# Optimization experiments

Hardware: AMD Instinct MI355X
Metric: run time of the kernel (lower is better)

## Reference

```python
import jax, jax.numpy as jnp
import numpy as np

T = 2_097_152  # timesteps


def setup_inputs() -> dict:
    key = jax.random.key(0)
    # precipitation P and potential evapotranspiration E, in mm/day
    x = jax.random.uniform(key, (T, 2), dtype=jnp.float32) * 10.0
    x1 = jnp.float32(350.0)  # production store capacity (mm)
    return {"x": x, "x1": x1}


def reference(x, x1):
    # GR4J production storage. s_init = 0.0.
    P = x[:, 0]
    E = x[:, 1]
    p_n = jax.nn.relu(P - E)  # net rainfall
    e_n = jax.nn.relu(E - P)  # net evapotranspiration
    # tanh(p_n/x1), tanh(e_n/x1) only depend on inputs -> precompute (same math)
    t_p = jnp.tanh(p_n / x1)
    t_e = jnp.tanh(e_n / x1)
    s0 = jnp.float32(0.0) * x1  # s_init * x1

    def step(s, te):
        tp, tn = te
        r = s / x1
        p_s = x1 * (1.0 - r ** 2) * tp / (1.0 + r * tp)
        e_s = s * (2.0 - r) * tn / (1.0 + (1.0 - r) * tn)
        s = s + p_s - e_s
        perc = s * (1.0 - (1.0 + ((4.0 / 9.0) * s / x1) ** 4) ** (-0.25))
        s = s - perc
        return s, (p_s, perc, s)

    _, (p_s, perc, s_store) = jax.lax.scan(step, s0, (t_p, t_e))

    # concat([p_n[:,None], e_n[:,None], p_s[:,None], perc[:,None]], axis=1)
    out = jnp.stack([p_n, e_n, p_s, perc], axis=1)  # [T, 4]
    # scale=True with mu/sigma None: standardize with batch statistics
    mu = jnp.mean(out, axis=0)
    sigma = jnp.std(out, axis=0)  # population std, matches tf.math.reduce_std
    out = (out - mu) / sigma
    return out, s_store[:, None]
```

## Files before the change

kernel.cpp:

```cpp
#include <hip/hip_runtime.h>


typedef float f32x4 __attribute__((ext_vector_type(4)));

#define LCH      64
#define CPB      128
#define TPB      256
#define BSTEPS   8192
#define WUP      1408
#define WUPAIR   704
#define WST      88
#define NPAIRW   4768
#define NCW      151
#define DASLOT   (32*NCW)
#define NCK      129
#define NMST     8

#define CC1 0.98078528f
#define CC2 0.92387953f
#define CC3 0.83146961f
#define CC4 0.70710678f
#define CC5 0.55557023f
#define CC6 0.38268343f
#define CC7 0.19509032f

__device__ __forceinline__ void stepk(float& s, const f32x4 k, float gma) {
    float s2m = s * s;
    float t1  = fmaf(k.y, s, k.x);
    float t2  = fmaf(k.w, s, k.z);
    float s1  = fmaf(s2m, t2, t1);
    float w2  = s1 * s1;
    float q4  = gma * s1;
    float w4  = w2 * w2;
    s = fmaf(-q4, w4, s1);
}

__device__ __forceinline__ void stepk_m(float& s, const f32x4 k, float gma,
                                        float& ps_o, float& pc_o) {
    float sp  = s;
    float s2m = s * s;
    float t1  = fmaf(k.y, s, k.x);
    float t2  = fmaf(k.w, s, k.z);
    float s1  = fmaf(s2m, t2, t1);
    float w2  = s1 * s1;
    float q4  = gma * s1;
    float w4  = w2 * w2;
    s = fmaf(-q4, w4, s1);
    ps_o = fmaxf(s1 - sp, 0.0f);
    pc_o = q4 * w4;
}

struct KC { float inv, x1, x1sq, x1_2, two_x1cu, five_x1sq, four_x1; };

__device__ __forceinline__ f32x4 mkk(float P, float Ev, const KC c,
                                     float& pn_o, float& en_o) {
    float d  = P - Ev;
    float pn = fmaxf(d, 0.f), en = fmaxf(-d, 0.f);
    float up = pn * c.inv, un = en * c.inv;
    float tp = up * fmaf(up * up, -(1.f/3.f), 1.f);
    float tn = un * fmaf(un * un, -(1.f/3.f), 1.f);
    float al = tp * c.inv, be = tn * c.inv;
    float a2 = al * al,  a3v = a2 * al;
    float b2 = be * be,  b3v = b2 * be;
    float e2 = fmaf(-be, c.x1, 1.f);
    float k0 = tp * c.x1;
    float k1 = 1.f - a2 * c.x1sq - (c.x1_2 * be * e2 + c.two_x1cu * b3v);
    float k2 = (a3v * c.x1sq - al) - (c.x1_2 * b2 - be * e2 - c.five_x1sq * b3v);
    float k3 = a2 + b2 - c.four_x1 * b3v;
    pn_o = pn; en_o = en;
    return (f32x4){k0, k1, k2, k3};
}

__global__ __launch_bounds__(256, 1) void scan_pair(
        const float* __restrict__ x, const float* __restrict__ x1p,
        f32x4* __restrict__ pspc4, f32x4* __restrict__ s4,
        float* __restrict__ partials) {
    __shared__ f32x4 smem[2 * DASLOT];
    __shared__ float red[32];
    f32x4* const dA = smem;
    f32x4* const dB = smem + DASLOT;
    f32x4* const tk = smem;

    const int tid  = threadIdx.x;
    const int lane = tid & 63;
    const int wid  = tid >> 6;
    const int b    = blockIdx.x;

    const float x1 = x1p[0];
    KC c;
    c.inv = 1.0f / x1; c.x1 = x1; c.x1sq = x1 * x1; c.x1_2 = 2.0f * x1;
    c.two_x1cu = 2.0f * x1 * c.x1sq; c.five_x1sq = 5.0f * c.x1sq;
    c.four_x1 = 4.0f * x1;
    const float gma = 64.0f / (6561.0f * c.x1sq * c.x1sq);
    const float cen = (184.0f / 350.0f) * x1;
    const float hw  = (208.0f / 350.0f) * x1;
    const float ihw = 1.0f / hw;

    float snode[8];
    {
        const float ND[8] = { CC1,  CC3,  CC5,  CC7, -CC7, -CC5, -CC3, -CC1};
        #pragma unroll
        for (int j = 0; j < 8; ++j) snode[j] = fmaf(hw, ND[j], cen);
    }
    f32x4 padA, padB;
    {
        const float qq = -2.0f * gma * ihw;
        const float c2_ = cen * cen, c3_ = c2_ * cen, c4_ = c2_ * c2_, c5_ = c4_ * cen;
        const float h2 = hw * hw, h3 = h2 * hw, h4 = h2 * h2, h5 = h4 * hw;
        padA = (f32x4){qq * c5_, fmaf(qq, 5.0f * hw * c4_, 1.0f),
                       qq * 10.0f * h2 * c3_, qq * 10.0f * h3 * c2_};
        padB = (f32x4){qq * 5.0f * h4 * cen, qq * h5, 0.0f, 0.0f};
    }

    {
        const f32x4* __restrict__ x4 = (const f32x4*)x;
        const long Bb = (long)b * 4096 - WUPAIR;
        const f32x4 z4 = (f32x4){0.f, 0.f, 0.f, 0.f};
        long g0 = Bb + tid;
        f32x4 w = (tid < NPAIRW && g0 >= 0) ? x4[g0] : z4;
        #pragma unroll 1
        for (int m = 0; m < 19; ++m) {
            const int p  = tid + (m << 8);
            const int p2 = p + 256;
            const long g  = Bb + p;
            const long g2 = Bb + p2;
            f32x4 wn = (p2 < NPAIRW && g2 >= 0) ? x4[g2] : z4;
            if (p < NPAIRW) {
                f32x4 ra, rb;
                if (g < 0) { ra = padA; rb = padB; }
                else {
                    float du0, du1;
                    const f32x4 kA = mkk(w.x, w.y, c, du0, du1);
                    const f32x4 kB = mkk(w.z, w.w, c, du0, du1);
                    float v[8];
                    #pragma unroll
                    for (int j = 0; j < 8; ++j) {
                        float s = snode[j];
                        stepk(s, kA, gma);
                        stepk(s, kB, gma);
                        v[j] = (s - cen) * ihw;
                    }
                    const float e0 = v[0] + v[7], e1 = v[1] + v[6];
                    const float e2 = v[2] + v[5], e3 = v[3] + v[4];
                    const float o0 = v[0] - v[7], o1 = v[1] - v[6];
                    const float o2 = v[2] - v[5], o3 = v[3] - v[4];
                    const float a0 = 0.125f * (e0 + e1 + e2 + e3);
                    const float a1 = 0.25f * (o0*CC1 + o1*CC3 + o2*CC5 + o3*CC7);
                    const float a2 = 0.25f * ((e0 - e3)*CC2 + (e1 - e2)*CC6);
                    const float a3 = 0.25f * (o0*CC3 - o1*CC7 - o2*CC1 - o3*CC5);
                    const float a4 = 0.25f * CC4 * ((e0 + e3) - (e1 + e2));
                    const float a5 = 0.25f * (o0*CC5 - o1*CC1 + o2*CC7 + o3*CC3);
                    const float a6 = 0.25f * ((e0 - e3)*CC6 - (e1 - e2)*CC2);
                    const float a7 = 0.25f * (o0*CC7 - o1*CC5 + o2*CC3 - o3*CC1);
                    ra = (f32x4){a0 - a2 + a4 - a6,
                                 a1 - 3.0f*a3 + 5.0f*a5 - 7.0f*a7,
                                 2.0f*a2 - 8.0f*a4 + 18.0f*a6,
                                 4.0f*a3 - 20.0f*a5 + 56.0f*a7};
                    rb = (f32x4){8.0f*a4 - 48.0f*a6,
                                 16.0f*a5 - 112.0f*a7,
                                 32.0f*a6,
                                 64.0f*a7};
                }
                const int slot = (p & 31) * NCW + (p >> 5);
                dA[slot] = ra;
                dB[slot] = rb;
            }
            w = wn;
        }
    }
    __syncthreads();

    float aps = 0.f, apc = 0.f, qps = 0.f, qpc = 0.f;
    float sg = 0.f;
    if (tid < CPB) {
        const int l = tid;
        const long chk = (long)b * CPB + l;
        const float s0 = (chk * LCH >= WUP) ? 0.47f * x1 : 0.0f;
        sg = (s0 - cen) * ihw;
        f32x4 PA[8], PB[8], QA[8], QB[8];
        auto rdw = [&](f32x4 (&A)[8], f32x4 (&B)[8], const int st) {
            const int jb = st << 3;
            const int base = (jb & 31) * NCW + l + (jb >> 5);
            #pragma unroll
            for (int u = 0; u < 8; ++u) A[u] = dA[base + u * NCW];
            #pragma unroll
            for (int u = 0; u < 8; ++u) B[u] = dB[base + u * NCW];
        };
        auto wstp = [&](f32x4 (&A)[8], f32x4 (&B)[8]) {
            #pragma unroll
            for (int u = 0; u < 8; ++u) {
                const float s2  = sg * sg;
                const float p0  = fmaf(A[u].y, sg, A[u].x);
                const float p1  = fmaf(A[u].w, sg, A[u].z);
                const float p2  = fmaf(B[u].y, sg, B[u].x);
                const float p3  = fmaf(B[u].w, sg, B[u].z);
                const float s4v = s2 * s2;
                const float q0  = fmaf(p1, s2, p0);
                const float q1  = fmaf(p3, s2, p2);
                sg = fmaf(q1, s4v, q0);
            }
        };
        rdw(PA, PB, 0);
        #pragma unroll 1
        for (int st = 0; st < WST; st += 2) {
            rdw(QA, QB, st + 1);
            wstp(PA, PB);
            rdw(PA, PB, st + 2);
            wstp(QA, QB);
        }
    }
    const float s_after = fmaf(hw, sg, cen);
    __syncthreads();

    float spn = 0.f, sen = 0.f, qpn = 0.f, qen = 0.f;
    {
        const f32x4* __restrict__ x4 = (const f32x4*)x;
        const long Fb = (long)b * 4096;
        f32x4 w = x4[Fb + tid];
        #pragma unroll 1
        for (int m = 0; m < 16; ++m) {
            const int f = tid + (m << 8);
            f32x4 wn = (m < 15) ? x4[Fb + f + 256] : w;
            #pragma unroll
            for (int h = 0; h < 2; ++h) {
                float pn, en;
                const f32x4 k = mkk(h ? w.z : w.x, h ? w.w : w.y, c, pn, en);
                const int t = 2 * f + h;
                tk[(t & 63) * NCK + (t >> 6)] = k;
                spn += pn; sen += en;
                qpn = fmaf(pn, pn, qpn); qen = fmaf(en, en, qen);
            }
            w = wn;
        }
    }
    __syncthreads();

    if (tid < CPB) {
        const int l = tid;
        const size_t chunk = (size_t)b * CPB + l;
        float s = s_after;
        f32x4 KP[8], KQ[8];
        auto rdk = [&](f32x4 (&K)[8], const int m) {
            const int base = (m << 3) * NCK + l;
            #pragma unroll
            for (int u = 0; u < 8; ++u) K[u] = tk[base + u * NCK];
        };
        auto mst = [&](f32x4 (&K)[8], const int m) {
            float psv[8], pcv[8], sv[8];
            #pragma unroll
            for (int u = 0; u < 8; ++u) {
                stepk_m(s, K[u], gma, psv[u], pcv[u]);
                sv[u] = s;
            }
            #pragma unroll
            for (int u = 0; u < 8; ++u) {
                aps += psv[u]; apc += pcv[u];
                qps = fmaf(psv[u], psv[u], qps); qpc = fmaf(pcv[u], pcv[u], qpc);
            }
            const size_t pb = chunk * 32 + 4 * m;
            pspc4[pb + 0] = (f32x4){psv[0], pcv[0], psv[1], pcv[1]};
            pspc4[pb + 1] = (f32x4){psv[2], pcv[2], psv[3], pcv[3]};
            pspc4[pb + 2] = (f32x4){psv[4], pcv[4], psv[5], pcv[5]};
            pspc4[pb + 3] = (f32x4){psv[6], pcv[6], psv[7], pcv[7]};
            const size_t sb = chunk * 16 + 2 * m;
            s4[sb]     = (f32x4){sv[0], sv[1], sv[2], sv[3]};
            s4[sb + 1] = (f32x4){sv[4], sv[5], sv[6], sv[7]};
        };
        rdk(KP, 0);
        #pragma unroll 1
        for (int m = 0; m < NMST; m += 2) {
            rdk(KQ, m + 1);
            mst(KP, m);
            rdk(KP, m + 2 < NMST ? m + 2 : NMST - 1);
            mst(KQ, m + 1);
        }
    }

    float vals[8] = {spn, sen, aps, apc, qpn, qen, qps, qpc};
    #pragma unroll
    for (int k = 0; k < 8; ++k) {
        float v = vals[k];
        #pragma unroll
        for (int off = 32; off > 0; off >>= 1) v += __shfl_down(v, off, 64);
        if (lane == 0) red[k * 4 + wid] = v;
    }
    __syncthreads();
    if (tid < 8)
        partials[b * 8 + tid] =
            red[tid * 4] + red[tid * 4 + 1] + red[tid * 4 + 2] + red[tid * 4 + 3];
}

__global__ __launch_bounds__(256) void normalize_stats(
        const float* __restrict__ x, const f32x4* __restrict__ pspc4,
        const float* __restrict__ pA, f32x4* __restrict__ out4,
        int nA, int Thalf, int T) {
    __shared__ float red[256];
    __shared__ float sst[8];
    const int tid = threadIdx.x;
    {
        const int c = tid & 7;
        float v = 0.f;
        for (int i = tid >> 3; i < nA; i += 32) v += pA[i * 8 + c];
        red[tid] = v;
        __syncthreads();
        for (int off = 128; off >= 8; off >>= 1) {
            if (tid < off) red[tid] += red[tid + off];
            __syncthreads();
        }
        if (tid == 0) {
            const float invT = 1.0f / (float)T;
            #pragma unroll
            for (int k = 0; k < 4; ++k) {
                float mu  = red[k] * invT;
                float var = fmaxf(fmaf(-mu, mu, red[4 + k] * invT), 0.0f);
                sst[k]     = mu;
                sst[4 + k] = (var > 0.0f) ? rsqrtf(var) : 0.0f;
            }
        }
        __syncthreads();
    }
    const float mu0 = sst[0], mu1 = sst[1], mu2 = sst[2], mu3 = sst[3];
    const float is0 = sst[4], is1 = sst[5], is2 = sst[6], is3 = sst[7];
    const f32x4* __restrict__ x4 = (const f32x4*)x;
    for (int i = blockIdx.x * 256 + tid; i < Thalf; i += 1024 * 256) {
        f32x4 xv = x4[i];
        f32x4 pq = pspc4[i];
        float d0 = xv.x - xv.y, d1 = xv.z - xv.w;
        out4[2 * i]     = (f32x4){(fmaxf(d0, 0.f) - mu0) * is0,
                                  (fmaxf(-d0, 0.f) - mu1) * is1,
                                  (pq.x - mu2) * is2,
                                  (pq.y - mu3) * is3};
        out4[2 * i + 1] = (f32x4){(fmaxf(d1, 0.f) - mu0) * is0,
                                  (fmaxf(-d1, 0.f) - mu1) * is1,
                                  (pq.z - mu2) * is2,
                                  (pq.w - mu3) * is3};
    }
}

#define L_CHUNK  128
#define FB_WARMUP 2048
__device__ __forceinline__ float inv1p_fb(float a) {
    float i1 = 1.0f - a;
    float i2 = fmaf(-a, i1, 1.0f);
    return fmaf(-a, i2, 1.0f);
}
struct SCfb { float x1, inv_x1, c49; };
__device__ __forceinline__ void scan_step_fb(float& s, float P, float E, const SCfb c,
                                             float& pn, float& en, float& ps, float& pc) {
    float d = P - E;
    float pn_ = fmaxf(d, 0.0f), en_ = fmaxf(-d, 0.0f);
    float up = pn_ * c.inv_x1;
    float tp = up * fmaf(up * up, -(1.0f / 3.0f), 1.0f);
    float un = en_ * c.inv_x1;
    float tn = un * fmaf(un * un, -(1.0f / 3.0f), 1.0f);
    float r = s * c.inv_x1;
    float ps_ = (tp * c.x1) * fmaf(-r, r, 1.0f) * inv1p_fb(r * tp);
    float es_ = (s * (2.0f - r)) * tn * inv1p_fb((1.0f - r) * tn);
    float s1 = s + ps_ - es_;
    float z = s1 * c.c49, z2 = z * z, v = z2 * z2;
    float t = fmaf(v, fmaf(v, 0.15625f, -0.25f), 1.0f);
    float s2 = s1 * t;
    pn = pn_; en = en_; ps = ps_; pc = s1 - s2; s = s2;
}
__global__ __launch_bounds__(256) void scan_kernel_fb(
        const float* __restrict__ x, const float* __restrict__ x1ptr,
        float* __restrict__ out, float* __restrict__ s_store,
        float* __restrict__ partials, int T) {
    const int c = blockIdx.x * blockDim.x + threadIdx.x;
    const int nchunks = (T + L_CHUNK - 1) / L_CHUNK;
    SCfb cc; cc.x1 = x1ptr[0]; cc.inv_x1 = 1.0f / cc.x1; cc.c49 = (4.0f / 9.0f) * cc.inv_x1;
    float s1a[4] = {0.f, 0.f, 0.f, 0.f};
    float s2a[4] = {0.f, 0.f, 0.f, 0.f};
    if (c < nchunks) {
        const int g0 = c * L_CHUNK;
        const int g1 = min(g0 + L_CHUNK, T);
        const int w0 = max(g0 - FB_WARMUP, 0);
        float s = 0.0f; float pn, en, ps, pc;
        const float2* __restrict__ x2 = (const float2*)x;
        for (int t = w0; t < g0; ++t) { float2 xv = x2[t]; scan_step_fb(s, xv.x, xv.y, cc, pn, en, ps, pc); }
        float4* __restrict__ out4 = (float4*)out;
        for (int t = g0; t < g1; ++t) {
            float2 xv = x2[t];
            scan_step_fb(s, xv.x, xv.y, cc, pn, en, ps, pc);
            out4[t] = make_float4(pn, en, ps, pc);
            s_store[t] = s;
            s1a[0] += pn; s1a[1] += en; s1a[2] += ps; s1a[3] += pc;
            s2a[0] = fmaf(pn, pn, s2a[0]); s2a[1] = fmaf(en, en, s2a[1]);
            s2a[2] = fmaf(ps, ps, s2a[2]); s2a[3] = fmaf(pc, pc, s2a[3]);
        }
    }
    __shared__ float red[256];
    float vals[8] = {s1a[0], s1a[1], s1a[2], s1a[3], s2a[0], s2a[1], s2a[2], s2a[3]};
    for (int k = 0; k < 8; ++k) {
        red[threadIdx.x] = vals[k];
        __syncthreads();
        for (int off = 128; off > 0; off >>= 1) {
            if ((int)threadIdx.x < off) red[threadIdx.x] += red[threadIdx.x + off];
            __syncthreads();
        }
        if (threadIdx.x == 0) partials[blockIdx.x * 8 + k] = red[0];
        __syncthreads();
    }
}
__global__ __launch_bounds__(64) void finalize_fb(
        const float* __restrict__ partials, float* __restrict__ stats, int nblk, int T) {
    const int lane = threadIdx.x;
    float v[8] = {0.f, 0.f, 0.f, 0.f, 0.f, 0.f, 0.f, 0.f};
    for (int b = lane; b < nblk; b += 64)
        for (int k = 0; k < 8; ++k) v[k] += partials[b * 8 + k];
    #pragma unroll
    for (int k = 0; k < 8; ++k)
        for (int off = 32; off > 0; off >>= 1) v[k] += __shfl_down(v[k], off, 64);
    if (lane == 0) {
        const float invT = 1.0f / (float)T;
        for (int k = 0; k < 4; ++k) {
            float mu = v[k] * invT;
            float var = fmaxf(fmaf(-mu, mu, v[k + 4] * invT), 0.0f);
            stats[k] = mu;
            stats[4 + k] = (var > 0.0f) ? rsqrtf(var) : 0.0f;
        }
    }
}
__global__ __launch_bounds__(256) void normalize_fb(
        float* __restrict__ out, const float* __restrict__ stats, int T) {
    const int t = blockIdx.x * blockDim.x + threadIdx.x;
    if (t >= T) return;
    const float4 mu = *(const float4*)stats;
    const float4 is = *(const float4*)(stats + 4);
    float4* o4 = (float4*)out;
    float4 v = o4[t];
    v.x = (v.x - mu.x) * is.x; v.y = (v.y - mu.y) * is.y;
    v.z = (v.z - mu.z) * is.z; v.w = (v.w - mu.w) * is.w;
    o4[t] = v;
}

extern "C" void kernel_launch(void* const* d_in, const int* in_sizes, int n_in,
                              void* d_out, int out_size, void* d_ws, size_t ws_size,
                              hipStream_t stream) {
    const float* x  = (const float*)d_in[0];
    const float* x1 = (const float*)d_in[1];
    const int T = in_sizes[0] / 2;

    float* out     = (float*)d_out;
    float* s_store = out + 4 * (size_t)T;

    const int nblk = T / BSTEPS;

    float* pA = (float*)d_ws;
    const size_t pq_off = 2048;
    const size_t need = (pq_off + 2 * (size_t)T) * sizeof(float);

    const bool fast = (T % BSTEPS == 0) && nblk >= 1 && nblk <= 256 &&
                      (ws_size >= need);

    if (fast) {
        f32x4* pspc4 = (f32x4*)((float*)d_ws + pq_off);
        scan_pair<<<nblk, TPB, 0, stream>>>(x, x1, pspc4, (f32x4*)s_store, pA);
        normalize_stats<<<1024, 256, 0, stream>>>(x, pspc4, pA,
                                                  (f32x4*)out, nblk, T / 2, T);
    } else {
        float* stats    = (float*)d_ws;
        float* partials = stats + 8;
        const int nchunks = (T + L_CHUNK - 1) / L_CHUNK;
        const int nblkA = (nchunks + 255) / 256;
        scan_kernel_fb<<<nblkA, 256, 0, stream>>>(x, x1, out, s_store, partials, T);
        finalize_fb<<<1, 64, 0, stream>>>(partials, stats, nblkA, T);
        normalize_fb<<<(T + 255) / 256, 256, 0, stream>>>(out, stats, T);
    }
}
```

Measured before the change: 127.8 us.

## Compose 16-step polynomial maps per thread, halve block size, fuse key building

Each thread now builds a polynomial transfer map over 16 timesteps (8 input pairs) instead of 2, evaluating 8 Chebyshev nodes through 16 steps and fitting a degree-7 map. The warm-up then walks far fewer composed maps (12 steps instead of 88). The block size is halved to 4096 steps with 32-step chunks and a 2-blocks-per-CU launch bound, giving more blocks. Building the per-step coefficients and the P/E statistics is fused into the map-construction pass, which removes a separate global read pass and a barrier. The risks are that a degree-7 fit over 16 nonlinear steps may lose accuracy, and the heavier per-thread work may create register pressure.

```diff
diff --git a/kernel.cpp b/kernel.cpp
--- a/kernel.cpp
+++ b/kernel.cpp
@@ -3,18 +3,17 @@
 
 typedef float f32x4 __attribute__((ext_vector_type(4)));
 
-#define LCH      64
+#define LCH      32
 #define CPB      128
 #define TPB      256
-#define BSTEPS   8192
-#define WUP      1408
-#define WUPAIR   704
-#define WST      88
-#define NPAIRW   4768
-#define NCW      151
-#define DASLOT   (32*NCW)
+#define BSTEPS   4096
+#define WUP      1536
+#define WUMAP    96
+#define WSTO     12
+#define NMAP     352
+#define HODD     176
 #define NCK      129
-#define NMST     8
+#define NMST     4
 
 #define CC1 0.98078528f
 #define CC2 0.92387953f
@@ -71,15 +70,14 @@
     return (f32x4){k0, k1, k2, k3};
 }
 
-__global__ __launch_bounds__(256, 1) void scan_pair(
+__global__ __launch_bounds__(256, 2) void scan_hexa(
         const float* __restrict__ x, const float* __restrict__ x1p,
         f32x4* __restrict__ pspc4, f32x4* __restrict__ s4,
         float* __restrict__ partials) {
-    __shared__ f32x4 smem[2 * DASLOT];
+    __shared__ f32x4 tk[32 * NCK];
+    __shared__ f32x4 mapA[NMAP];
+    __shared__ f32x4 mapB[NMAP];
     __shared__ float red[32];
-    f32x4* const dA = smem;
-    f32x4* const dB = smem + DASLOT;
-    f32x4* const tk = smem;
 
     const int tid  = threadIdx.x;
     const int lane = tid & 63;
@@ -102,71 +100,82 @@
         #pragma unroll
         for (int j = 0; j < 8; ++j) snode[j] = fmaf(hw, ND[j], cen);
     }
-    f32x4 padA, padB;
-    {
-        const float qq = -2.0f * gma * ihw;
-        const float c2_ = cen * cen, c3_ = c2_ * cen, c4_ = c2_ * c2_, c5_ = c4_ * cen;
-        const float h2 = hw * hw, h3 = h2 * hw, h4 = h2 * h2, h5 = h4 * hw;
-        padA = (f32x4){qq * c5_, fmaf(qq, 5.0f * hw * c4_, 1.0f),
-                       qq * 10.0f * h2 * c3_, qq * 10.0f * h3 * c2_};
-        padB = (f32x4){qq * 5.0f * h4 * cen, qq * h5, 0.0f, 0.0f};
-    }
+
+    float spn = 0.f, sen = 0.f, qpn = 0.f, qen = 0.f;
 
     {
         const f32x4* __restrict__ x4 = (const f32x4*)x;
-        const long Bb = (long)b * 4096 - WUPAIR;
         const f32x4 z4 = (f32x4){0.f, 0.f, 0.f, 0.f};
-        long g0 = Bb + tid;
-        f32x4 w = (tid < NPAIRW && g0 >= 0) ? x4[g0] : z4;
-        #pragma unroll 1
-        for (int m = 0; m < 19; ++m) {
-            const int p  = tid + (m << 8);
-            const int p2 = p + 256;
-            const long g  = Bb + p;
-            const long g2 = Bb + p2;
-            f32x4 wn = (p2 < NPAIRW && g2 >= 0) ? x4[g2] : z4;
-            if (p < NPAIRW) {
-                f32x4 ra, rb;
-                if (g < 0) { ra = padA; rb = padB; }
-                else {
-                    float du0, du1;
-                    const f32x4 kA = mkk(w.x, w.y, c, du0, du1);
-                    const f32x4 kB = mkk(w.z, w.w, c, du0, du1);
-                    float v[8];
-                    #pragma unroll
-                    for (int j = 0; j < 8; ++j) {
-                        float s = snode[j];
-                        stepk(s, kA, gma);
-                        stepk(s, kB, gma);
-                        v[j] = (s - cen) * ihw;
-                    }
-                    const float e0 = v[0] + v[7], e1 = v[1] + v[6];
-                    const float e2 = v[2] + v[5], e3 = v[3] + v[4];
-                    const float o0 = v[0] - v[7], o1 = v[1] - v[6];
-                    const float o2 = v[2] - v[5], o3 = v[3] - v[4];
-                    const float a0 = 0.125f * (e0 + e1 + e2 + e3);
-                    const float a1 = 0.25f * (o0*CC1 + o1*CC3 + o2*CC5 + o3*CC7);
-                    const float a2 = 0.25f * ((e0 - e3)*CC2 + (e1 - e2)*CC6);
-                    const float a3 = 0.25f * (o0*CC3 - o1*CC7 - o2*CC1 - o3*CC5);
-                    const float a4 = 0.25f * CC4 * ((e0 + e3) - (e1 + e2));
-                    const float a5 = 0.25f * (o0*CC5 - o1*CC1 + o2*CC7 + o3*CC3);
-                    const float a6 = 0.25f * ((e0 - e3)*CC6 - (e1 - e2)*CC2);
-                    const float a7 = 0.25f * (o0*CC7 - o1*CC5 + o2*CC3 - o3*CC1);
-                    ra = (f32x4){a0 - a2 + a4 - a6,
-                                 a1 - 3.0f*a3 + 5.0f*a5 - 7.0f*a7,
-                                 2.0f*a2 - 8.0f*a4 + 18.0f*a6,
-                                 4.0f*a3 - 20.0f*a5 + 56.0f*a7};
-                    rb = (f32x4){8.0f*a4 - 48.0f*a6,
-                                 16.0f*a5 - 112.0f*a7,
-                                 32.0f*a6,
-                                 64.0f*a7};
+
+        auto build = [&](const int mi, f32x4 (&w)[8]) {
+            const int m = mi - WUMAP;
+            float sv[8];
+            #pragma unroll
+            for (int j = 0; j < 8; ++j) sv[j] = snode[j];
+            const bool mainm = (m >= 0);
+            #pragma unroll
+            for (int q = 0; q < 8; ++q) {
+                float pn0, en0, pn1, en1;
+                const f32x4 kA = mkk(w[q].x, w[q].y, c, pn0, en0);
+                const f32x4 kB = mkk(w[q].z, w[q].w, c, pn1, en1);
+                #pragma unroll
+                for (int j = 0; j < 8; ++j) {
+                    stepk(sv[j], kA, gma);
+                    stepk(sv[j], kB, gma);
                 }
-                const int slot = (p & 31) * NCW + (p >> 5);
-                dA[slot] = ra;
-                dB[slot] = rb;
+                if (mainm) {
+                    spn += pn0 + pn1; sen += en0 + en1;
+                    qpn = fmaf(pn0, pn0, fmaf(pn1, pn1, qpn));
+                    qen = fmaf(en0, en0, fmaf(en1, en1, qen));
+                    const int t = 16 * m + 2 * q;
+                    const int r = t & 31, col = t >> 5;
+                    tk[r * NCK + col]       = kA;
+                    tk[(r + 1) * NCK + col] = kB;
+                }
             }
-            w = wn;
-        }
+            float v[8];
+            #pragma unroll
+            for (int j = 0; j < 8; ++j) v[j] = (sv[j] - cen) * ihw;
+            const float e0 = v[0] + v[7], e1 = v[1] + v[6];
+            const float e2 = v[2] + v[5], e3 = v[3] + v[4];
+            const float o0 = v[0] - v[7], o1 = v[1] - v[6];
+            const float o2 = v[2] - v[5], o3 = v[3] - v[4];
+            const float a0 = 0.125f * (e0 + e1 + e2 + e3);
+            const float a1 = 0.25f * (o0*CC1 + o1*CC3 + o2*CC5 + o3*CC7);
+            const float a2 = 0.25f * ((e0 - e3)*CC2 + (e1 - e2)*CC6);
+            const float a3 = 0.25f * (o0*CC3 - o1*CC7 - o2*CC1 - o3*CC5);
+            const float a4 = 0.25f * CC4 * ((e0 + e3) - (e1 + e2));
+            const float a5 = 0.25f * (o0*CC5 - o1*CC1 + o2*CC7 + o3*CC3);
+            const float a6 = 0.25f * ((e0 - e3)*CC6 - (e1 - e2)*CC2);
+            const float a7 = 0.25f * (o0*CC7 - o1*CC5 + o2*CC3 - o3*CC1);
+            const f32x4 ra = (f32x4){a0 - a2 + a4 - a6,
+                                     a1 - 3.0f*a3 + 5.0f*a5 - 7.0f*a7,
+                                     2.0f*a2 - 8.0f*a4 + 18.0f*a6,
+                                     4.0f*a3 - 20.0f*a5 + 56.0f*a7};
+            const f32x4 rb = (f32x4){8.0f*a4 - 48.0f*a6,
+                                     16.0f*a5 - 112.0f*a7,
+                                     32.0f*a6,
+                                     64.0f*a7};
+            const int slot = (mi >> 1) + ((mi & 1) ? HODD : 0);
+            mapA[slot] = ra;
+            mapB[slot] = rb;
+        };
+
+        const long base = (long)b * (BSTEPS / 2);
+        f32x4 wa[8], wb[8];
+        const long gpA = base + 8L * (tid - WUMAP);
+        #pragma unroll
+        for (int q = 0; q < 8; ++q) {
+            const long g = gpA + q;
+            wa[q] = (g >= 0) ? x4[g] : z4;
+        }
+        const bool hasB = (tid < NMAP - 256);
+        const long gpB = base + 8L * (tid + 256 - WUMAP);
+        #pragma unroll
+        for (int q = 0; q < 8; ++q)
+            wb[q] = hasB ? x4[gpB + q] : z4;
+        build(tid, wa);
+        if (hasB) build(tid + 256, wb);
     }
     __syncthreads();
 
@@ -174,17 +183,18 @@
     float sg = 0.f;
     if (tid < CPB) {
         const int l = tid;
-        const long chk = (long)b * CPB + l;
-        const float s0 = (chk * LCH >= WUP) ? 0.47f * x1 : 0.0f;
+        const long gstart = ((long)b * CPB + l) * LCH;
+        const float s0 = (gstart >= WUP) ? 0.47f * x1 : 0.0f;
         sg = (s0 - cen) * ihw;
         f32x4 PA[8], PB[8], QA[8], QB[8];
         auto rdw = [&](f32x4 (&A)[8], f32x4 (&B)[8], const int st) {
-            const int jb = st << 3;
-            const int base = (jb & 31) * NCW + l + (jb >> 5);
-            #pragma unroll
-            for (int u = 0; u < 8; ++u) A[u] = dA[base + u * NCW];
-            #pragma unroll
-            for (int u = 0; u < 8; ++u) B[u] = dB[base + u * NCW];
+            const int base = l + 4 * st;
+            #pragma unroll
+            for (int u = 0; u < 8; ++u)
+                A[u] = mapA[base + (u >> 1) + ((u & 1) ? HODD : 0)];
+            #pragma unroll
+            for (int u = 0; u < 8; ++u)
+                B[u] = mapB[base + (u >> 1) + ((u & 1) ? HODD : 0)];
         };
         auto wstp = [&](f32x4 (&A)[8], f32x4 (&B)[8]) {
             #pragma unroll
@@ -202,38 +212,14 @@
         };
         rdw(PA, PB, 0);
         #pragma unroll 1
-        for (int st = 0; st < WST; st += 2) {
+        for (int st = 0; st < WSTO; st += 2) {
             rdw(QA, QB, st + 1);
             wstp(PA, PB);
-            rdw(PA, PB, st + 2);
+            rdw(PA, PB, st + 2 < WSTO ? st + 2 : WSTO - 1);
             wstp(QA, QB);
         }
     }
     const float s_after = fmaf(hw, sg, cen);
-    __syncthreads();
-
-    float spn = 0.f, sen = 0.f, qpn = 0.f, qen = 0.f;
-    {
-        const f32x4* __restrict__ x4 = (const f32x4*)x;
-        const long Fb = (long)b * 4096;
-        f32x4 w = x4[Fb + tid];
-        #pragma unroll 1
-        for (int m = 0; m < 16; ++m) {
-            const int f = tid + (m << 8);
-            f32x4 wn = (m < 15) ? x4[Fb + f + 256] : w;
-            #pragma unroll
-            for (int h = 0; h < 2; ++h) {
-                float pn, en;
-                const f32x4 k = mkk(h ? w.z : w.x, h ? w.w : w.y, c, pn, en);
-                const int t = 2 * f + h;
-                tk[(t & 63) * NCK + (t >> 6)] = k;
-                spn += pn; sen += en;
-                qpn = fmaf(pn, pn, qpn); qen = fmaf(en, en, qen);
-            }
-            w = wn;
-        }
-    }
-    __syncthreads();
 
     if (tid < CPB) {
         const int l = tid;
@@ -257,12 +243,12 @@
                 aps += psv[u]; apc += pcv[u];
                 qps = fmaf(psv[u], psv[u], qps); qpc = fmaf(pcv[u], pcv[u], qpc);
             }
-            const size_t pb = chunk * 32 + 4 * m;
+            const size_t pb = chunk * 16 + 4 * m;
             pspc4[pb + 0] = (f32x4){psv[0], pcv[0], psv[1], pcv[1]};
             pspc4[pb + 1] = (f32x4){psv[2], pcv[2], psv[3], pcv[3]};
             pspc4[pb + 2] = (f32x4){psv[4], pcv[4], psv[5], pcv[5]};
             pspc4[pb + 3] = (f32x4){psv[6], pcv[6], psv[7], pcv[7]};
-            const size_t sb = chunk * 16 + 2 * m;
+            const size_t sb = chunk * 8 + 2 * m;
             s4[sb]     = (f32x4){sv[0], sv[1], sv[2], sv[3]};
             s4[sb + 1] = (f32x4){sv[4], sv[5], sv[6], sv[7]};
         };
@@ -447,15 +433,15 @@
     const int nblk = T / BSTEPS;
 
     float* pA = (float*)d_ws;
-    const size_t pq_off = 2048;
+    const size_t pq_off = 4608;
     const size_t need = (pq_off + 2 * (size_t)T) * sizeof(float);
 
-    const bool fast = (T % BSTEPS == 0) && nblk >= 1 && nblk <= 256 &&
+    const bool fast = (T % BSTEPS == 0) && nblk >= 1 && nblk <= 512 &&
                       (ws_size >= need);
 
     if (fast) {
         f32x4* pspc4 = (f32x4*)((float*)d_ws + pq_off);
-        scan_pair<<<nblk, TPB, 0, stream>>>(x, x1, pspc4, (f32x4*)s_store, pA);
+        scan_hexa<<<nblk, TPB, 0, stream>>>(x, x1, pspc4, (f32x4*)s_store, pA);
         normalize_stats<<<1024, 256, 0, stream>>>(x, pspc4, pA,
                                                   (f32x4*)out, nblk, T / 2, T);
     } else {
```

Measured after the change: 111.1 us. -13.1%, faster.
